# Optimization experiments

Hardware: AMD Instinct MI355X
Metric: run time of the kernel (lower is better)

## Reference

```python
import jax, jax.numpy as jnp
import numpy as np

MODEL_DIM = 1024
NUM_HEADS = 16
K_DIM = MODEL_DIM // NUM_HEADS


def setup_inputs() -> dict:
    key = jax.random.key(0)
    kx, kw1, kw2 = jax.random.split(key, 3)
    B, L, D = 4, 2048, MODEL_DIM
    x = jax.random.normal(kx, (B, L, D), dtype=jnp.float32)
    # nn.Linear(D, 3D, bias=False): y = x @ W^T; store transposed form [D, 3D]
    scale1 = 1.0 / np.sqrt(D)
    Wqkv = jax.random.uniform(kw1, (D, 3 * D), dtype=jnp.float32, minval=-scale1, maxval=scale1)
    Wout = jax.random.uniform(kw2, (D, D), dtype=jnp.float32, minval=-scale1, maxval=scale1)
    return {"x": x, "Wqkv": Wqkv, "Wout": Wout}


def reference(x, Wqkv, Wout):
    B, L, D = x.shape
    H, Kd = NUM_HEADS, K_DIM
    qkv = x @ Wqkv  # [B, L, 3D]
    q, k, v = jnp.split(qkv, 3, axis=-1)

    def heads(t):  # [B, L, D] -> [B, H, L, Kd]
        return t.reshape(B, L, H, Kd).transpose(0, 2, 1, 3)

    qh, kh, vh = heads(q), heads(k), heads(v)
    scores = jnp.einsum('bhqd,bhkd->bhqk', qh, kh) / jnp.sqrt(jnp.float32(Kd))
    causal = jnp.triu(jnp.ones((L, L), dtype=bool), k=1)  # True above diagonal
    scores = jnp.where(causal, -jnp.inf, scores)
    probs = jax.nn.softmax(scores, axis=-1)
    attended = jnp.einsum('bhqk,bhkd->bhqd', probs, vh)
    concatted = attended.transpose(0, 2, 1, 3).reshape(B, L, D)
    # dropout is identity in eval mode
    return concatted @ Wout
```

## Files before the change

kernel.cpp:

```cpp
#include <hip/hip_runtime.h>

typedef unsigned short u16;
typedef unsigned int   u32;
typedef __bf16   bf16x8 __attribute__((ext_vector_type(8)));
typedef float    f32x4  __attribute__((ext_vector_type(4)));
typedef u16      u16x4  __attribute__((ext_vector_type(4)));
typedef u16      u16x8  __attribute__((ext_vector_type(8)));
typedef u32      u32x2  __attribute__((ext_vector_type(2)));

__device__ __forceinline__ u16 f2bf(float f) {
    unsigned u = __float_as_uint(f);
    u += 0x7FFFu + ((u >> 16) & 1u);
    return (u16)(u >> 16);
}

__device__ __forceinline__ u32 pack_bf16(float a, float b) {
#if __has_builtin(__builtin_amdgcn_cvt_pk_bf16_f32)
    typedef __bf16 bf16x2 __attribute__((ext_vector_type(2)));
    bf16x2 r = __builtin_amdgcn_cvt_pk_bf16_f32(a, b);
    return __builtin_bit_cast(u32, r);
#else
    return (u32)f2bf(a) | ((u32)f2bf(b) << 16);
#endif
}

__device__ __forceinline__ void async_copy16(const u16* g, u16* l) {
    __builtin_amdgcn_global_load_lds(
        (const __attribute__((address_space(1))) unsigned*)g,
        (__attribute__((address_space(3))) unsigned*)l, 16, 0, 0);
}

__device__ __forceinline__ bf16x8 lds_frag(const u16* p) {
    return *(const bf16x8*)p;
}

__global__ __launch_bounds__(256) void conv_bf16(const float* __restrict__ x,
                                                 u16* __restrict__ xb) {
    size_t i = ((size_t)blockIdx.x * 256 + threadIdx.x) * 4;
    float4 v = *(const float4*)(x + i);
    u16x4 o = { f2bf(v.x), f2bf(v.y), f2bf(v.z), f2bf(v.w) };
    *(u16x4*)(xb + i) = o;
}

__global__ __launch_bounds__(256) void transpose_cvt(const float* __restrict__ W,
                                                     u16* __restrict__ Wt,
                                                     int Kd, int Nd) {
    __shared__ u16 t[64 * 72];
    const int tid = threadIdx.x;
    const int n0 = blockIdx.x * 64, k0 = blockIdx.y * 64;
#pragma unroll
    for (int i = 0; i < 4; ++i) {
        int lin = i * 256 + tid;
        int kr = lin >> 4, nc = (lin & 15) << 2;
        float4 v = *(const float4*)(W + (size_t)(k0 + kr) * Nd + n0 + nc);
        u16x4 o = { f2bf(v.x), f2bf(v.y), f2bf(v.z), f2bf(v.w) };
        *(u16x4*)&t[kr * 72 + nc] = o;
    }
    __syncthreads();
#pragma unroll
    for (int i = 0; i < 2; ++i) {
        int lin = i * 256 + tid;
        int nr = lin >> 3, kc = (lin & 7) << 3;
        u16x8 o;
#pragma unroll
        for (int jj = 0; jj < 8; ++jj) o[jj] = t[(kc + jj) * 72 + nr];
        *(u16x8*)(Wt + (size_t)(n0 + nr) * Kd + k0 + kc) = o;
    }
}

template <bool QKV>
__global__ __launch_bounds__(256) void gemm_bt(const u16* __restrict__ A,
                                               const u16* __restrict__ Bt,
                                               u16* __restrict__ outb,
                                               float* __restrict__ outf,
                                               int K, int N) {
    __shared__ u16 As[128 * 32];
    __shared__ u16 Bs[128 * 32];
    const int tid = threadIdx.x;
    const int lane = tid & 63;
    const int wv = tid >> 6;
    const int wr = (wv >> 1) * 64;
    const int wc = (wv & 1) * 64;
    const int qd = lane >> 4;
    const int c  = lane & 15;
    const int m0 = blockIdx.y * 128;
    const int n0 = blockIdx.x * 128;

    const int srow = tid >> 2;
    const int scol = (tid & 3) << 3;

    f32x4 acc[4][4] = {};

    for (int k0 = 0; k0 < K; k0 += 32) {
        __syncthreads();
        async_copy16(A  + (size_t)(m0 +      srow) * K + k0 + scol, &As[tid * 8]);
        async_copy16(A  + (size_t)(m0 + 64 + srow) * K + k0 + scol, &As[2048 + tid * 8]);
        async_copy16(Bt + (size_t)(n0 +      srow) * K + k0 + scol, &Bs[tid * 8]);
        async_copy16(Bt + (size_t)(n0 + 64 + srow) * K + k0 + scol, &Bs[2048 + tid * 8]);
        __syncthreads();

        bf16x8 af[4], bf[4];
#pragma unroll
        for (int i = 0; i < 4; ++i) af[i] = lds_frag(&As[(wr + i * 16 + c) * 32 + qd * 8]);
#pragma unroll
        for (int j = 0; j < 4; ++j) bf[j] = lds_frag(&Bs[(wc + j * 16 + c) * 32 + qd * 8]);
#pragma unroll
        for (int i = 0; i < 4; ++i)
#pragma unroll
            for (int j = 0; j < 4; ++j)
                acc[i][j] = __builtin_amdgcn_mfma_f32_16x16x32_bf16(af[i], bf[j], acc[i][j], 0, 0, 0);
    }

#pragma unroll
    for (int i = 0; i < 4; ++i)
#pragma unroll
        for (int j = 0; j < 4; ++j) {
            if constexpr (QKV) {
                int n = n0 + wc + j * 16 + c;
                int which = n >> 10, h = (n >> 6) & 15, kd = n & 63;
                int m_base = m0 + wr + i * 16 + qd * 4;
                int b = m_base >> 11, l0 = m_base & 2047;
                int bh = b * 16 + h;
                if (which == 2) {
                    u32x2 o2;
                    o2[0] = pack_bf16(acc[i][j][0], acc[i][j][1]);
                    o2[1] = pack_bf16(acc[i][j][2], acc[i][j][3]);
                    *(u32x2*)(outb + (size_t)(128 + bh) * 131072 + (size_t)kd * 2048 + l0) = o2;
                } else if (which == 0) {
#pragma unroll
                    for (int r = 0; r < 4; ++r)
                        outb[(size_t)bh * 131072 + (size_t)(l0 + r) * 64 + kd] =
                            f2bf(acc[i][j][r] * 0.1803368801f);
                } else {
#pragma unroll
                    for (int r = 0; r < 4; ++r)
                        outb[(size_t)(64 + bh) * 131072 + (size_t)(l0 + r) * 64 + kd] =
                            f2bf(acc[i][j][r]);
                }
            } else {
#pragma unroll
                for (int r = 0; r < 4; ++r) {
                    int m = m0 + wr + i * 16 + qd * 4 + r;
                    int n = n0 + wc + j * 16 + c;
                    outf[(size_t)m * N + n] = acc[i][j][r];
                }
            }
        }
}

__global__ __launch_bounds__(512, 4) void attn_kernel(const u16* __restrict__ qkv,
                                                      u16* __restrict__ att) {
    __shared__ u16 Ks[128 * 64];
    __shared__ u16 Vt[64 * 128];
    __shared__ u16 Ps[8][16 * 136];

    const int tid = threadIdx.x;
    const int lane = tid & 63;
    const int w = tid >> 6;
    const int qd = lane >> 4;
    const int c = lane & 15;

    const int flat = blockIdx.x + 8 * blockIdx.y;
    const int bh = (flat & 7) + 8 * ((flat >> 3) & 7);
    const int bx = flat >> 6;
    const int b = bh >> 4, h = bh & 15;

    const u16* Qg = qkv + (size_t)bh * 131072;
    const u16* Kg = qkv + (size_t)(64 + bh) * 131072;
    const u16* Vg = qkv + (size_t)(128 + bh) * 131072;

    u32 k_go[2], v_go[2];
    u16 *k_ld[2], *v_ld[2];
#pragma unroll
    for (int it = 0; it < 2; ++it) {
        int lin = it * 512 + tid;
        int krw = lin >> 3, kch = lin & 7;
        k_go[it] = krw * 64 + ((kch ^ (krw & 7)) << 3);
        k_ld[it] = &Ks[lin * 8];
        int vrw = lin >> 4, vch = lin & 15;
        v_go[it] = vrw * 2048 + ((vch ^ (vrw & 15)) << 3);
        v_ld[it] = &Vt[lin * 8];
    }
    const u16* kb[2];
#pragma unroll
    for (int ks = 0; ks < 2; ++ks)
        kb[ks] = &Ks[c * 64 + (((ks * 4 + qd) ^ (c & 7)) << 3)];
    const u16* vb[4];
#pragma unroll
    for (int kc = 0; kc < 4; ++kc)
        vb[kc] = &Vt[c * 128 + (((kc * 4 + qd) ^ c) << 3)];
    u16* ps_w = &Ps[w][c * 136 + qd * 4];
    const u16* ps_r = &Ps[w][c * 136 + qd * 8];

#pragma unroll
    for (int seg = 0; seg < 2; ++seg) {
        const int qt = seg ? (15 - bx) : bx;
        const int qrow = qt * 128 + w * 16 + c;

        bf16x8 qf[2];
        qf[0] = *(const bf16x8*)(Qg + (size_t)qrow * 64 + qd * 8);
        qf[1] = *(const bf16x8*)(Qg + (size_t)qrow * 64 + 32 + qd * 8);

        f32x4 acc[4] = {};
        float m_run = -1e30f, l_run = 0.0f;

        const int nkt = qt + 1;
        for (int kt = 0; kt < nkt; ++kt) {
            __syncthreads();
#pragma unroll
            for (int it = 0; it < 2; ++it) {
                async_copy16(Kg + (size_t)kt * 8192 + k_go[it], k_ld[it]);
                async_copy16(Vg + (size_t)kt * 128  + v_go[it], v_ld[it]);
            }
            __syncthreads();

            f32x4 s[8] = {};
#pragma unroll
            for (int ks = 0; ks < 2; ++ks)
#pragma unroll
                for (int f = 0; f < 8; ++f) {
                    bf16x8 kf = lds_frag(kb[ks] + f * 1024);
                    s[f] = __builtin_amdgcn_mfma_f32_16x16x32_bf16(kf, qf[ks], s[f], 0, 0, 0);
                }

            if (kt == qt) {
#pragma unroll
                for (int f = 0; f < 8; ++f)
#pragma unroll
                    for (int r = 0; r < 4; ++r) {
                        int key = kt * 128 + f * 16 + qd * 4 + r;
                        if (key > qrow) s[f][r] = -3e38f;
                    }
            }

            float mloc = -3e38f;
#pragma unroll
            for (int f = 0; f < 8; ++f) {
                float a0 = fmaxf(s[f][0], s[f][1]), a1 = fmaxf(s[f][2], s[f][3]);
                mloc = fmaxf(mloc, fmaxf(a0, a1));
            }
            mloc = fmaxf(mloc, __shfl_xor(mloc, 16, 64));
            mloc = fmaxf(mloc, __shfl_xor(mloc, 32, 64));

            float mnew = fmaxf(m_run, mloc);
            float alpha = exp2f(m_run - mnew);
            m_run = mnew;

            float rs = 0.0f;
#pragma unroll
            for (int f = 0; f < 8; ++f)
#pragma unroll
                for (int r = 0; r < 4; ++r) {
                    float p = exp2f(s[f][r] - mnew);
                    s[f][r] = p;
                    rs += p;
                }
            rs += __shfl_xor(rs, 16, 64);
            rs += __shfl_xor(rs, 32, 64);
            l_run = l_run * alpha + rs;
#pragma unroll
            for (int jo = 0; jo < 4; ++jo)
#pragma unroll
                for (int r = 0; r < 4; ++r) acc[jo][r] *= alpha;

#pragma unroll
            for (int f = 0; f < 8; ++f) {
                u32x2 pw;
                pw[0] = pack_bf16(s[f][0], s[f][1]);
                pw[1] = pack_bf16(s[f][2], s[f][3]);
                *(u32x2*)(ps_w + f * 16) = pw;
            }

#pragma unroll
            for (int kc = 0; kc < 4; ++kc) {
                bf16x8 pf = lds_frag(ps_r + kc * 32);
#pragma unroll
                for (int jo = 0; jo < 4; ++jo) {
                    bf16x8 vf = lds_frag(vb[kc] + jo * 2048);
                    acc[jo] = __builtin_amdgcn_mfma_f32_16x16x32_bf16(vf, pf, acc[jo], 0, 0, 0);
                }
            }
        }

        float inv = 1.0f / l_run;
        u16* arow = att + ((size_t)b * 2048 + qrow) * 1024 + h * 64;
#pragma unroll
        for (int jo = 0; jo < 4; ++jo) {
            u32x2 o2;
            o2[0] = pack_bf16(acc[jo][0] * inv, acc[jo][1] * inv);
            o2[1] = pack_bf16(acc[jo][2] * inv, acc[jo][3] * inv);
            *(u32x2*)(arow + jo * 16 + qd * 4) = o2;
        }
    }
}

extern "C" void kernel_launch(void* const* d_in, const int* in_sizes, int n_in,
                              void* d_out, int out_size, void* d_ws, size_t ws_size,
                              hipStream_t stream) {
    const float* x    = (const float*)d_in[0];
    const float* Wqkv = (const float*)d_in[1];
    const float* Wout = (const float*)d_in[2];
    float* out = (float*)d_out;

    char* ws = (char*)d_ws;
    u16* x_bf   = (u16*)(ws);
    u16* wqkv_t = (u16*)(ws + 16777216);
    u16* wout_t = (u16*)(ws + 23068672);
    u16* qkv_h  = (u16*)(ws + 25165824);
    u16* att    = (u16*)(ws + 75497472);

    conv_bf16<<<dim3(8192), dim3(256), 0, stream>>>(x, x_bf);
    transpose_cvt<<<dim3(48, 16), dim3(256), 0, stream>>>(Wqkv, wqkv_t, 1024, 3072);
    transpose_cvt<<<dim3(16, 16), dim3(256), 0, stream>>>(Wout, wout_t, 1024, 1024);
    gemm_bt<true ><<<dim3(24, 64), dim3(256), 0, stream>>>(x_bf, wqkv_t, qkv_h, nullptr, 1024, 3072);
    attn_kernel<<<dim3(8, 64), dim3(512), 0, stream>>>(qkv_h, att);
    gemm_bt<false><<<dim3(8, 64), dim3(256), 0, stream>>>(att, wout_t, nullptr, out, 1024, 1024);
}
```

Baseline: 288.2 us.

## Double-buffer K/V tiles and process two query groups per wave in attention

The attention kernel drops to 4 waves per block, and each wave now handles 32 query rows as two 16-row groups. Every K and V fragment read from LDS feeds two MFMAs. K/V tiles are double-buffered in LDS, so the next tile's async copy is issued before computing on the current one, removing the second barrier per iteration. The P staging buffer gets an XOR-swizzled layout, and exp2 and the final reciprocal use hardware intrinsics. In exchange, register pressure rises, LDS use per block grows, and fewer waves are resident to hide latency.

Result: faster. 273.4 us (-5.2%).

```diff
diff --git a/kernel.cpp b/kernel.cpp
--- a/kernel.cpp
+++ b/kernel.cpp
@@ -7,6 +7,13 @@
 typedef u16      u16x4  __attribute__((ext_vector_type(4)));
 typedef u16      u16x8  __attribute__((ext_vector_type(8)));
 typedef u32      u32x2  __attribute__((ext_vector_type(2)));
+typedef u32      u32x4  __attribute__((ext_vector_type(4)));
+
+#if __has_builtin(__builtin_amdgcn_exp2f)
+#define EXP2(x) __builtin_amdgcn_exp2f(x)
+#else
+#define EXP2(x) exp2f(x)
+#endif
 
 __device__ __forceinline__ u16 f2bf(float f) {
     unsigned u = __float_as_uint(f);
@@ -148,11 +155,11 @@
         }
 }
 
-__global__ __launch_bounds__(512, 4) void attn_kernel(const u16* __restrict__ qkv,
+__global__ __launch_bounds__(256, 2) void attn_kernel(const u16* __restrict__ qkv,
                                                       u16* __restrict__ att) {
-    __shared__ u16 Ks[128 * 64];
-    __shared__ u16 Vt[64 * 128];
-    __shared__ u16 Ps[8][16 * 136];
+    __shared__ u16 Ks[2][128 * 64];
+    __shared__ u16 Vt[2][64 * 128];
+    __shared__ u16 Ps[4][16 * 128];
 
     const int tid = threadIdx.x;
     const int lane = tid & 63;
@@ -169,59 +176,79 @@
     const u16* Kg = qkv + (size_t)(64 + bh) * 131072;
     const u16* Vg = qkv + (size_t)(128 + bh) * 131072;
 
-    u32 k_go[2], v_go[2];
-    u16 *k_ld[2], *v_ld[2];
-#pragma unroll
-    for (int it = 0; it < 2; ++it) {
-        int lin = it * 512 + tid;
+    u32 k_go[4], v_go[4], s_lo[4];
+#pragma unroll
+    for (int it = 0; it < 4; ++it) {
+        int lin = it * 256 + tid;
         int krw = lin >> 3, kch = lin & 7;
         k_go[it] = krw * 64 + ((kch ^ (krw & 7)) << 3);
-        k_ld[it] = &Ks[lin * 8];
         int vrw = lin >> 4, vch = lin & 15;
         v_go[it] = vrw * 2048 + ((vch ^ (vrw & 15)) << 3);
-        v_ld[it] = &Vt[lin * 8];
-    }
-    const u16* kb[2];
+        s_lo[it] = lin * 8;
+    }
+
+    u32 kf_off[2];
 #pragma unroll
     for (int ks = 0; ks < 2; ++ks)
-        kb[ks] = &Ks[c * 64 + (((ks * 4 + qd) ^ (c & 7)) << 3)];
-    const u16* vb[4];
+        kf_off[ks] = c * 64 + (((ks * 4 + qd) ^ (c & 7)) << 3);
+    u32 vf_off[4];
 #pragma unroll
     for (int kc = 0; kc < 4; ++kc)
-        vb[kc] = &Vt[c * 128 + (((kc * 4 + qd) ^ c) << 3)];
-    u16* ps_w = &Ps[w][c * 136 + qd * 4];
-    const u16* ps_r = &Ps[w][c * 136 + qd * 8];
+        vf_off[kc] = c * 128 + (((kc * 4 + qd) ^ c) << 3);
+    u16* psw = &Ps[w][c * 128 + (qd & 1) * 4];
+    const u16* psr = &Ps[w][c * 128];
 
 #pragma unroll
     for (int seg = 0; seg < 2; ++seg) {
         const int qt = seg ? (15 - bx) : bx;
-        const int qrow = qt * 128 + w * 16 + c;
-
-        bf16x8 qf[2];
-        qf[0] = *(const bf16x8*)(Qg + (size_t)qrow * 64 + qd * 8);
-        qf[1] = *(const bf16x8*)(Qg + (size_t)qrow * 64 + 32 + qd * 8);
-
-        f32x4 acc[4] = {};
-        float m_run = -1e30f, l_run = 0.0f;
+        const int qa_row = qt * 128 + w * 32 + c;
+        const int qb_row = qa_row + 16;
+
+        bf16x8 qa[2], qb[2];
+#pragma unroll
+        for (int ks = 0; ks < 2; ++ks) {
+            qa[ks] = *(const bf16x8*)(Qg + (size_t)qa_row * 64 + ks * 32 + qd * 8);
+            qb[ks] = *(const bf16x8*)(Qg + (size_t)qb_row * 64 + ks * 32 + qd * 8);
+        }
+
+        f32x4 acca[4] = {}, accb[4] = {};
+        float m_a = -1e30f, l_a = 0.0f, m_b = -1e30f, l_b = 0.0f;
 
         const int nkt = qt + 1;
+        int p = 0;
         for (int kt = 0; kt < nkt; ++kt) {
             __syncthreads();
-#pragma unroll
-            for (int it = 0; it < 2; ++it) {
-                async_copy16(Kg + (size_t)kt * 8192 + k_go[it], k_ld[it]);
-                async_copy16(Vg + (size_t)kt * 128  + v_go[it], v_ld[it]);
-            }
-            __syncthreads();
-
-            f32x4 s[8] = {};
-#pragma unroll
-            for (int ks = 0; ks < 2; ++ks)
+            if (kt == 0) {
+#pragma unroll
+                for (int it = 0; it < 4; ++it) {
+                    async_copy16(Kg + (size_t)kt * 8192 + k_go[it], &Ks[0][s_lo[it]]);
+                    async_copy16(Vg + (size_t)kt * 128  + v_go[it], &Vt[0][s_lo[it]]);
+                }
+                __syncthreads();
+            }
+            if (kt + 1 < nkt) {
+                const int nt = kt + 1, np = p ^ 1;
+#pragma unroll
+                for (int it = 0; it < 4; ++it) {
+                    async_copy16(Kg + (size_t)nt * 8192 + k_go[it], &Ks[np][s_lo[it]]);
+                    async_copy16(Vg + (size_t)nt * 128  + v_go[it], &Vt[np][s_lo[it]]);
+                }
+            }
+
+            const u16* ksb = Ks[p];
+            const u16* vtb = Vt[p];
+
+            f32x4 sa[8] = {}, sb[8] = {};
+#pragma unroll
+            for (int ks = 0; ks < 2; ++ks) {
+                const u16* kp = ksb + kf_off[ks];
 #pragma unroll
                 for (int f = 0; f < 8; ++f) {
-                    bf16x8 kf = lds_frag(kb[ks] + f * 1024);
-                    s[f] = __builtin_amdgcn_mfma_f32_16x16x32_bf16(kf, qf[ks], s[f], 0, 0, 0);
-                }
+                    bf16x8 kf = lds_frag(kp + f * 1024);
+                    sa[f] = __builtin_amdgcn_mfma_f32_16x16x32_bf16(kf, qa[ks], sa[f], 0, 0, 0);
+                    sb[f] = __builtin_amdgcn_mfma_f32_16x16x32_bf16(kf, qb[ks], sb[f], 0, 0, 0);
+                }
+            }
 
             if (kt == qt) {
 #pragma unroll
@@ -229,67 +256,96 @@
 #pragma unroll
                     for (int r = 0; r < 4; ++r) {
                         int key = kt * 128 + f * 16 + qd * 4 + r;
-                        if (key > qrow) s[f][r] = -3e38f;
+                        if (key > qa_row) sa[f][r] = -3e38f;
+                        if (key > qb_row) sb[f][r] = -3e38f;
                     }
             }
 
-            float mloc = -3e38f;
+            float ma = -3e38f, mb = -3e38f;
 #pragma unroll
             for (int f = 0; f < 8; ++f) {
-                float a0 = fmaxf(s[f][0], s[f][1]), a1 = fmaxf(s[f][2], s[f][3]);
-                mloc = fmaxf(mloc, fmaxf(a0, a1));
-            }
-            mloc = fmaxf(mloc, __shfl_xor(mloc, 16, 64));
-            mloc = fmaxf(mloc, __shfl_xor(mloc, 32, 64));
-
-            float mnew = fmaxf(m_run, mloc);
-            float alpha = exp2f(m_run - mnew);
-            m_run = mnew;
-
-            float rs = 0.0f;
+                ma = fmaxf(ma, fmaxf(fmaxf(sa[f][0], sa[f][1]), fmaxf(sa[f][2], sa[f][3])));
+                mb = fmaxf(mb, fmaxf(fmaxf(sb[f][0], sb[f][1]), fmaxf(sb[f][2], sb[f][3])));
+            }
+            ma = fmaxf(ma, __shfl_xor(ma, 16, 64));
+            ma = fmaxf(ma, __shfl_xor(ma, 32, 64));
+            mb = fmaxf(mb, __shfl_xor(mb, 16, 64));
+            mb = fmaxf(mb, __shfl_xor(mb, 32, 64));
+
+            float mna = fmaxf(m_a, ma), mnb = fmaxf(m_b, mb);
+            float ala = EXP2(m_a - mna), alb = EXP2(m_b - mnb);
+            m_a = mna; m_b = mnb;
+
+            float ra = 0.0f, rb = 0.0f;
 #pragma unroll
             for (int f = 0; f < 8; ++f)
 #pragma unroll
                 for (int r = 0; r < 4; ++r) {
-                    float p = exp2f(s[f][r] - mnew);
-                    s[f][r] = p;
-                    rs += p;
-                }
-            rs += __shfl_xor(rs, 16, 64);
-            rs += __shfl_xor(rs, 32, 64);
-            l_run = l_run * alpha + rs;
+                    float pa = EXP2(sa[f][r] - mna);
+                    float pb = EXP2(sb[f][r] - mnb);
+                    sa[f][r] = pa; sb[f][r] = pb;
+                    ra += pa; rb += pb;
+                }
+            ra += __shfl_xor(ra, 16, 64);
+            ra += __shfl_xor(ra, 32, 64);
+            rb += __shfl_xor(rb, 16, 64);
+            rb += __shfl_xor(rb, 32, 64);
+            l_a = l_a * ala + ra;
+            l_b = l_b * alb + rb;
 #pragma unroll
             for (int jo = 0; jo < 4; ++jo)
 #pragma unroll
-                for (int r = 0; r < 4; ++r) acc[jo][r] *= alpha;
-
+                for (int r = 0; r < 4; ++r) { acca[jo][r] *= ala; accb[jo][r] *= alb; }
+
+            u32x4 pfa[4], pfb[4];
 #pragma unroll
             for (int f = 0; f < 8; ++f) {
                 u32x2 pw;
-                pw[0] = pack_bf16(s[f][0], s[f][1]);
-                pw[1] = pack_bf16(s[f][2], s[f][3]);
-                *(u32x2*)(ps_w + f * 16) = pw;
-            }
+                pw[0] = pack_bf16(sa[f][0], sa[f][1]);
+                pw[1] = pack_bf16(sa[f][2], sa[f][3]);
+                *(u32x2*)(psw + (((f * 2 + (qd >> 1)) ^ c) << 3)) = pw;
+            }
+#pragma unroll
+            for (int kc = 0; kc < 4; ++kc)
+                pfa[kc] = *(const u32x4*)(psr + (((kc * 4 + qd) ^ c) << 3));
+#pragma unroll
+            for (int f = 0; f < 8; ++f) {
+                u32x2 pw;
+                pw[0] = pack_bf16(sb[f][0], sb[f][1]);
+                pw[1] = pack_bf16(sb[f][2], sb[f][3]);
+                *(u32x2*)(psw + (((f * 2 + (qd >> 1)) ^ c) << 3)) = pw;
+            }
+#pragma unroll
+            for (int kc = 0; kc < 4; ++kc)
+                pfb[kc] = *(const u32x4*)(psr + (((kc * 4 + qd) ^ c) << 3));
 
 #pragma unroll
             for (int kc = 0; kc < 4; ++kc) {
-                bf16x8 pf = lds_frag(ps_r + kc * 32);
+                const u16* vp = vtb + vf_off[kc];
+                bf16x8 pa = __builtin_bit_cast(bf16x8, pfa[kc]);
+                bf16x8 pb = __builtin_bit_cast(bf16x8, pfb[kc]);
 #pragma unroll
                 for (int jo = 0; jo < 4; ++jo) {
-                    bf16x8 vf = lds_frag(vb[kc] + jo * 2048);
-                    acc[jo] = __builtin_amdgcn_mfma_f32_16x16x32_bf16(vf, pf, acc[jo], 0, 0, 0);
-                }
-            }
+                    bf16x8 vf = lds_frag(vp + jo * 2048);
+                    acca[jo] = __builtin_amdgcn_mfma_f32_16x16x32_bf16(vf, pa, acca[jo], 0, 0, 0);
+                    accb[jo] = __builtin_amdgcn_mfma_f32_16x16x32_bf16(vf, pb, accb[jo], 0, 0, 0);
+                }
+            }
+            p ^= 1;
         }
 
-        float inv = 1.0f / l_run;
-        u16* arow = att + ((size_t)b * 2048 + qrow) * 1024 + h * 64;
+        float ia = __builtin_amdgcn_rcpf(l_a), ib = __builtin_amdgcn_rcpf(l_b);
+        u16* ar = att + ((size_t)b * 2048 + qa_row) * 1024 + h * 64;
+        u16* br = att + ((size_t)b * 2048 + qb_row) * 1024 + h * 64;
 #pragma unroll
         for (int jo = 0; jo < 4; ++jo) {
-            u32x2 o2;
-            o2[0] = pack_bf16(acc[jo][0] * inv, acc[jo][1] * inv);
-            o2[1] = pack_bf16(acc[jo][2] * inv, acc[jo][3] * inv);
-            *(u32x2*)(arow + jo * 16 + qd * 4) = o2;
+            u32x2 oa, ob;
+            oa[0] = pack_bf16(acca[jo][0] * ia, acca[jo][1] * ia);
+            oa[1] = pack_bf16(acca[jo][2] * ia, acca[jo][3] * ia);
+            ob[0] = pack_bf16(accb[jo][0] * ib, accb[jo][1] * ib);
+            ob[1] = pack_bf16(accb[jo][2] * ib, accb[jo][3] * ib);
+            *(u32x2*)(ar + jo * 16 + qd * 4) = oa;
+            *(u32x2*)(br + jo * 16 + qd * 4) = ob;
         }
     }
 }
@@ -313,6 +369,6 @@
     transpose_cvt<<<dim3(48, 16), dim3(256), 0, stream>>>(Wqkv, wqkv_t, 1024, 3072);
     transpose_cvt<<<dim3(16, 16), dim3(256), 0, stream>>>(Wout, wout_t, 1024, 1024);
     gemm_bt<true ><<<dim3(24, 64), dim3(256), 0, stream>>>(x_bf, wqkv_t, qkv_h, nullptr, 1024, 3072);
-    attn_kernel<<<dim3(8, 64), dim3(512), 0, stream>>>(qkv_h, att);
+    attn_kernel<<<dim3(8, 64), dim3(256), 0, stream>>>(qkv_h, att);
     gemm_bt<false><<<dim3(8, 64), dim3(256), 0, stream>>>(att, wout_t, nullptr, out, 1024, 1024);
 }
```
